# Kernel optimization log

Measured on AMD Instinct MI355X. Metric: run time of the kernel, lower is better.

The kernel has to match this reference:

```python
import jax, jax.numpy as jnp
import numpy as np

OMEGA = 0.3        # self.omega
NU = 0.2           # self.nu
LAMBDA_DECAY = 0.1 # lambda_decay
MU_INIT = 0.25     # nn.Parameter init
EPS_DENOM = 1e-8
EPS_SQRT = 1e-24   # safe sqrt (avoids nan grad at exactly-zero distance)


def setup_inputs() -> dict:
    key = jax.random.key(0)
    k1, k2, k3, k4 = jax.random.split(key, 4)
    T, D = 4096, 896  # seq_len, Qwen2.5-0.5B hidden size
    return {
        "hidden_states": jax.random.normal(k1, (T, D), dtype=jnp.float32),
        "m_t": jax.random.uniform(k2, (T,), dtype=jnp.float32),
        "c_t": jax.random.uniform(k3, (T,), dtype=jnp.float32),
        "d_t": jax.random.uniform(k4, (T,), dtype=jnp.float32),
        "mu": jnp.asarray(MU_INIT, dtype=jnp.float32),
    }


def _semantic_drift(hidden_states, m_t, c_t, d_t, mu):
    T, D = hidden_states.shape
    # F.normalize(h, p=2, dim=1): x / max(||x||, eps)
    norms = jnp.linalg.norm(hidden_states, axis=1, keepdims=True)
    h = hidden_states / jnp.maximum(norms, 1e-12)          # [T, D]

    # Causal decayed-softmax anchor: alpha[t, s] over s <= t
    sim = jnp.einsum("td,sd->ts", h, h)                    # [T, T], h(s)^T h(t) at row t
    idx = jnp.arange(T)
    tds = (idx[:, None] - idx[None, :]).astype(jnp.float32)  # t - s
    causal = tds >= 0.0
    sqrt_d = jnp.sqrt(jnp.asarray(D, jnp.float32))
    denom = sqrt_d * jnp.exp(LAMBDA_DECAY * tds) + EPS_DENOM
    logits = jnp.where(causal, sim / denom, -jnp.inf)
    alpha = jax.nn.softmax(logits, axis=1)                 # [T, T]
    g = jnp.einsum("ts,sd->td", alpha, h)                  # h_global(t), [T, D]

    # dist(h(t), h_global(t)) — normalize_hidden=True, so plain euclidean norm
    dist = jnp.sqrt(jnp.maximum(jnp.sum((h - g) ** 2, axis=1), EPS_SQRT))  # [T]

    # dist_max(t) = max_{s<=t} ||h(s) - h_global(t)|| (torch loop starts max at 0)
    hn2 = jnp.sum(h * h, axis=1)                           # [T]
    gn2 = jnp.sum(g * g, axis=1)                           # [T]
    cross = jnp.einsum("td,sd->ts", g, h)                  # g(t)·h(s)
    d2 = jnp.maximum(hn2[None, :] - 2.0 * cross + gn2[:, None], EPS_SQRT)
    dmat = jnp.sqrt(d2)                                    # [T, T], dist(h(s), g(t))
    dist_max = jnp.max(jnp.where(causal, dmat, 0.0), axis=1)
    dist_max = jnp.where(dist_max < 1e-6, 1.0, dist_max)

    dist_ratio = dist / (dist_max + EPS_DENOM)
    stability = 1.0 - OMEGA * c_t + NU * d_t
    xi = 1.0 - mu * m_t
    return jnp.clip(dist_ratio * stability * xi, 0.0, 1.0)  # [T]


def reference(hidden_states, m_t, c_t, d_t, mu):
    return _semantic_drift(hidden_states, m_t, c_t, d_t, mu)
```

## Files before the change

### kernel.cpp

```cpp
#include <hip/hip_runtime.h>
#include <math.h>


#define T_ 4096
#define D_ 896
#define TP (T_ + 64)

typedef float f32x4 __attribute__((ext_vector_type(4)));
typedef unsigned short u16x8 __attribute__((ext_vector_type(8)));
typedef __bf16 bf16x8 __attribute__((ext_vector_type(8)));

union V16 { uint4 u; u16x8 v; };

__device__ __forceinline__ u16x8 ld16(const unsigned short* p) {
  V16 x; x.u = *(const uint4*)p; return x.v;
}
__device__ __forceinline__ void st16(unsigned short* p, u16x8 v) {
  V16 x; x.v = v; *(uint4*)p = x.u;
}
__device__ __forceinline__ unsigned short f2bf(float f) {
  unsigned int u = __float_as_uint(f);
  u += 0x7FFFu + ((u >> 16) & 1u);
  return (unsigned short)(u >> 16);
}
__device__ __forceinline__ float bf2f(unsigned short b) {
  return __uint_as_float(((unsigned int)b) << 16);
}
__device__ __forceinline__ float4 bf4f(uint2 u) {
  return make_float4(bf2f((unsigned short)(u.x & 0xffff)),
                     bf2f((unsigned short)(u.x >> 16)),
                     bf2f((unsigned short)(u.y & 0xffff)),
                     bf2f((unsigned short)(u.y >> 16)));
}
__device__ __forceinline__ f32x4 mfma16(u16x8 a, u16x8 b, f32x4 c) {
  return __builtin_amdgcn_mfma_f32_16x16x32_bf16(
      __builtin_bit_cast(bf16x8, a), __builtin_bit_cast(bf16x8, b), c, 0, 0, 0);
}

typedef __attribute__((address_space(1))) const void glob_cv;
typedef __attribute__((address_space(3))) void lds_v;
__device__ __forceinline__ void gload16(const void* g, void* l) {
  __builtin_amdgcn_global_load_lds((glob_cv*)g, (lds_v*)l, 16, 0, 0);
}

__device__ __forceinline__ void stage32(const unsigned short* __restrict__ g0,
                                        int stride, unsigned short* lds0, int tid) {
  #pragma unroll
  for (int it = 0; it < 2; ++it) {
    const int e = it * 256 + tid;
    const int row = e >> 3, pg = e & 7;
    const int gg = pg ^ (row & 7);
    gload16(g0 + (size_t)row * stride + gg * 8, lds0 + e * 8);
  }
}

__device__ __forceinline__ void tri2_decode(int b, int& ti, int& sj) {
  int p = (int)((sqrtf(4.0f * (float)b + 1.0f) - 1.0f) * 0.5f);
  while ((p + 1) * (p + 2) <= b) ++p;
  while (p * (p + 1) > b) --p;
  const int r = b - p * (p + 1);
  if (r >= p + 1) { ti = 2 * p + 1; sj = r - (p + 1); }
  else            { ti = 2 * p;     sj = r; }
}

__global__ __launch_bounds__(256) void k_prep(const float* __restrict__ x,
    float* __restrict__ invnorm, unsigned short* __restrict__ hb) {
  const int t = (int)blockIdx.x, tid = (int)threadIdx.x;
  const int c = tid * 4;
  float4 v = make_float4(0.f, 0.f, 0.f, 0.f);
  float s = 0.f;
  if (c < D_) {
    v = *(const float4*)(x + (size_t)t * D_ + c);
    s = v.x * v.x + v.y * v.y + v.z * v.z + v.w * v.w;
  }
  __shared__ float sb[4];
  __shared__ float sinv;
  #pragma unroll
  for (int off = 32; off > 0; off >>= 1) s += __shfl_down(s, off, 64);
  if ((tid & 63) == 0) sb[tid >> 6] = s;
  __syncthreads();
  if (tid == 0) {
    const float tot = sb[0] + sb[1] + sb[2] + sb[3];
    const float iv = 1.0f / fmaxf(sqrtf(tot), 1e-12f);
    invnorm[t] = iv; sinv = iv;
  }
  __syncthreads();
  if (c < D_) {
    const float iv = sinv;
    *(ushort4*)(hb + (size_t)t * D_ + c) = make_ushort4(
        f2bf(v.x * iv), f2bf(v.y * iv), f2bf(v.z * iv), f2bf(v.w * iv));
  }
}

__global__ __launch_bounds__(256) void k_transp(const unsigned short* __restrict__ hb,
                                                unsigned short* __restrict__ hbTp) {
  __shared__ unsigned short Ts[32][36];
  const int t0 = (int)blockIdx.x * 32, d0 = (int)blockIdx.y * 32;
  const int r = (int)threadIdx.x >> 3, c = ((int)threadIdx.x & 7) * 4;
  const ushort4 v = *(const ushort4*)(hb + (size_t)(t0 + r) * D_ + d0 + c);
  Ts[r][c] = v.x; Ts[r][c + 1] = v.y; Ts[r][c + 2] = v.z; Ts[r][c + 3] = v.w;
  __syncthreads();
  const ushort4 o = make_ushort4(Ts[c][r], Ts[c + 1][r], Ts[c + 2][r], Ts[c + 3][r]);
  *(ushort4*)(hbTp + (size_t)(d0 + r) * TP + 32 + t0 + c) = o;
  if (blockIdx.x == 0)
    *(ushort4*)(hbTp + (size_t)(d0 + r) * TP + c) = make_ushort4(0, 0, 0, 0);
}

__global__ __launch_bounds__(256) void k_sega(const unsigned short* __restrict__ hb,
                                              float* __restrict__ Sseg) {
  const int seg = (int)blockIdx.x, tid = (int)threadIdx.x;
  const int wv = tid >> 6, lane = tid & 63;
  __shared__ float4 part[4][56];
  const int c = (int)blockIdx.y * 224 + lane * 4;
  float4 acc = make_float4(0.f, 0.f, 0.f, 0.f);
  if (lane < 56) {
    #pragma unroll
    for (int r = 0; r < 8; ++r) {
      const int row = seg * 32 + wv * 8 + r;
      const float4 h = bf4f(*(const uint2*)(hb + (size_t)row * D_ + c));
      acc.x += h.x; acc.y += h.y; acc.z += h.z; acc.w += h.w;
    }
    part[wv][lane] = acc;
  }
  __syncthreads();
  if (wv == 0 && lane < 56) {
    const float4 a = part[0][lane], b = part[1][lane];
    const float4 d = part[2][lane], e = part[3][lane];
    *(float4*)(Sseg + (size_t)seg * D_ + c) = make_float4(
        a.x + b.x + d.x + e.x, a.y + b.y + d.y + e.y,
        a.z + b.z + d.z + e.z, a.w + b.w + d.w + e.w);
  }
}

__global__ __launch_bounds__(256) void k_segb(const float* __restrict__ Sseg,
                                              float* __restrict__ Eseg) {
  const int tid = (int)threadIdx.x;
  const int wv = tid >> 6, lane = tid & 63;
  const int c = (int)blockIdx.x * 4 + wv;
  float v0 = Sseg[(size_t)lane * D_ + c];
  float v1 = Sseg[(size_t)(64 + lane) * D_ + c];
  const float o0 = v0, o1 = v1;
  #pragma unroll
  for (int off = 1; off < 64; off <<= 1) {
    const float n0 = __shfl_up(v0, off, 64);
    const float n1 = __shfl_up(v1, off, 64);
    if (lane >= off) { v0 += n0; v1 += n1; }
  }
  const float tot0 = __shfl(v0, 63, 64);
  Eseg[(size_t)lane * D_ + c] = v0 - o0;
  Eseg[(size_t)(64 + lane) * D_ + c] = v1 - o1 + tot0;
}

__global__ __launch_bounds__(64) void k_segc(const unsigned short* __restrict__ hb,
    const float* __restrict__ Eseg, float* __restrict__ P) {
  const int seg = (int)blockIdx.x, tid = (int)threadIdx.x;
  if (tid >= 56) return;
  const int c = (int)blockIdx.y * 224 + tid * 4;
  float4 run = *(const float4*)(Eseg + (size_t)seg * D_ + c);
  for (int r = 0; r < 32; ++r) {
    const int row = seg * 32 + r;
    const float4 h = bf4f(*(const uint2*)(hb + (size_t)row * D_ + c));
    run.x += h.x; run.y += h.y; run.z += h.z; run.w += h.w;
    *(float4*)(P + (size_t)row * D_ + c) = run;
  }
}

__global__ __launch_bounds__(256) void k_bandw(const unsigned short* __restrict__ hb,
    unsigned short* __restrict__ wband, float* __restrict__ invLb) {
  const int t0 = (int)blockIdx.x * 16;
  const int tid = (int)threadIdx.x;
  const int wv = tid >> 6, lane = tid & 63;
  const int tcol = lane & 15, quad = lane >> 4;
  __shared__ float sims[16][52];
  if (wv < 3) {
    const int s_base = t0 - 32 + wv * 16;
    if (s_base + 15 >= 0) {
      const int srow = max(s_base + tcol, 0);
      f32x4 acc = {};
      const unsigned short* arow = hb + (size_t)srow * D_ + quad * 8;
      const unsigned short* brow = hb + (size_t)(t0 + tcol) * D_ + quad * 8;
      #pragma unroll 1
      for (int c4 = 0; c4 < 4; ++c4) {
        u16x8 av[7], bv[7];
        #pragma unroll
        for (int i = 0; i < 7; ++i) {
          av[i] = ld16(arow + (c4 * 7 + i) * 32);
          bv[i] = ld16(brow + (c4 * 7 + i) * 32);
        }
        #pragma unroll
        for (int i = 0; i < 7; ++i) acc = mfma16(av[i], bv[i], acc);
      }
      #pragma unroll
      for (int r = 0; r < 4; ++r)
        sims[tcol][wv * 16 + quad * 4 + r] = acc[r];
    }
  }
  __syncthreads();
  if (wv == 0) {
    u16x8 af0, af1;
    float lsum = 0.f;
    #pragma unroll
    for (int j = 0; j < 8; ++j) {
      {
        const int k = quad * 8 + j;
        const int dt = tcol + 32 - k;
        const int s = t0 - 32 + k;
        unsigned short wb = 0;
        if (dt < 32 && s >= 0)
          wb = f2bf(__expf(sims[tcol][k] * (__expf(-0.1f * (float)dt) * 0.033407657f)));
        af0[j] = wb;
        lsum += bf2f(wb);
      }
      {
        const int k = 32 + quad * 8 + j;
        const int dt = tcol + 32 - k;
        unsigned short wb = 0;
        if (dt >= 0)
          wb = f2bf(__expf(sims[tcol][k] * (__expf(-0.1f * (float)dt) * 0.033407657f)));
        af1[j] = wb;
        lsum += bf2f(wb);
      }
    }
    lsum += __shfl_xor(lsum, 16, 64);
    lsum += __shfl_xor(lsum, 32, 64);
    st16(wband + (size_t)(t0 + tcol) * 64 + quad * 8, af0);
    st16(wband + (size_t)(t0 + tcol) * 64 + 32 + quad * 8, af1);
    if (lane < 16) {
      const int t = t0 + lane;
      invLb[t] = 1.0f / (lsum + ((t >= 32) ? (float)(t - 31) : 0.f));
    }
  }
}

__global__ __launch_bounds__(256) void k_bandg(const unsigned short* __restrict__ hbTp,
    const unsigned short* __restrict__ wband, const float* __restrict__ invLb,
    const float* __restrict__ P, const float* __restrict__ x,
    const float* __restrict__ invnorm, unsigned short* __restrict__ gb,
    float* __restrict__ gn2, float* __restrict__ dist2) {
  const int t0 = (int)blockIdx.x * 16;
  const int by = (int)blockIdx.y;
  const int tid = (int)threadIdx.x;
  const int wv = tid >> 6, lane = tid & 63;
  const int tcol = lane & 15, quad = lane >> 4;
  const u16x8 af0 = ld16(wband + (size_t)(t0 + tcol) * 64 + quad * 8);
  const u16x8 af1 = ld16(wband + (size_t)(t0 + tcol) * 64 + 32 + quad * 8);
  float invLr[4], inrr[4];
  #pragma unroll
  for (int r = 0; r < 4; ++r) {
    const int tt = t0 + quad * 4 + r;
    invLr[r] = invLb[tt];
    inrr[r]  = invnorm[tt];
  }
  float sgl[4] = {0.f, 0.f, 0.f, 0.f}, sdl[4] = {0.f, 0.f, 0.f, 0.f};
  for (int i = wv; i < 7; i += 4) {
    const int d = (by * 7 + i) * 16 + tcol;
    const unsigned short* brow = hbTp + (size_t)d * TP + t0 + quad * 8;
    const u16x8 b0 = ld16(brow);
    const u16x8 b1 = ld16(brow + 32);
    f32x4 C = {};
    C = mfma16(af0, b0, C);
    C = mfma16(af1, b1, C);
    #pragma unroll
    for (int r = 0; r < 4; ++r) {
      const int tt = t0 + quad * 4 + r;
      float gacc = C[r];
      if (tt >= 32) gacc += P[(size_t)(tt - 32) * D_ + d];
      const float g = gacc * invLr[r];
      gb[(size_t)tt * D_ + d] = f2bf(g);
      const float e = x[(size_t)tt * D_ + d] * inrr[r] - g;
      sgl[r] += g * g;
      sdl[r] += e * e;
    }
  }
  #pragma unroll
  for (int r = 0; r < 4; ++r) {
    float sg = sgl[r], sd = sdl[r];
    sg += __shfl_xor(sg, 1, 64); sg += __shfl_xor(sg, 2, 64);
    sg += __shfl_xor(sg, 4, 64); sg += __shfl_xor(sg, 8, 64);
    sd += __shfl_xor(sd, 1, 64); sd += __shfl_xor(sd, 2, 64);
    sd += __shfl_xor(sd, 4, 64); sd += __shfl_xor(sd, 8, 64);
    if (tcol == 0) {
      atomicAdd(&gn2[t0 + quad * 4 + r], sg);
      atomicAdd(&dist2[t0 + quad * 4 + r], sd);
    }
  }
}

__global__ __launch_bounds__(256, 5) void k_gemm3(const unsigned short* __restrict__ gb,
    const unsigned short* __restrict__ hb, const float* __restrict__ gn2,
    unsigned int* __restrict__ dmaxu) {
  const int bswz = ((int)blockIdx.x & 7) * 132 + ((int)blockIdx.x >> 3);
  int ti, sj;
  tri2_decode(bswz, ti, sj);
  const int t0 = ti * 64, s0 = sj * 128;
  __shared__ unsigned short As[64 * 64];
  __shared__ unsigned short Bs[128 * 64];
  __shared__ unsigned int dmx[64];
  const int tid = (int)threadIdx.x;
  const int lane = tid & 63, wv = tid >> 6;
  const int tcol = lane & 15, quad = lane >> 4;
  if (tid < 64) dmx[tid] = 0u;
  f32x4 acc[4][2] = {};

  for (int kc = 0; kc < 14; ++kc) {
    __syncthreads();
    stage32(gb + (size_t)t0 * D_ + kc * 64, D_, As, tid);
    stage32(hb + (size_t)s0 * D_ + kc * 64, D_, Bs, tid);
    stage32(hb + (size_t)(s0 + 64) * D_ + kc * 64, D_, Bs + 64 * 64, tid);
    __syncthreads();
    #pragma unroll
    for (int ks = 0; ks < 2; ++ks) {
      const int go = ((ks * 4 + quad) ^ (tcol & 7)) * 8;
      u16x8 bf[2], af[4];
      #pragma unroll
      for (int ni = 0; ni < 2; ++ni)
        bf[ni] = ld16(&Bs[(wv * 32 + ni * 16 + tcol) * 64 + go]);
      #pragma unroll
      for (int mi = 0; mi < 4; ++mi)
        af[mi] = ld16(&As[(mi * 16 + tcol) * 64 + go]);
      #pragma unroll
      for (int mi = 0; mi < 4; ++mi)
        #pragma unroll
        for (int ni = 0; ni < 2; ++ni)
          acc[mi][ni] = mfma16(af[mi], bf[ni], acc[mi][ni]);
    }
  }

  #pragma unroll
  for (int mi = 0; mi < 4; ++mi) {
    #pragma unroll
    for (int r = 0; r < 4; ++r) {
      const int t = t0 + mi * 16 + quad * 4 + r;
      const float gn = gn2[t];
      float m2 = 0.f;
      #pragma unroll
      for (int ni = 0; ni < 2; ++ni) {
        const int s = s0 + wv * 32 + ni * 16 + tcol;
        if (t >= s)
          m2 = fmaxf(m2, fmaxf(1.0f - 2.0f * acc[mi][ni][r] + gn, 1e-24f));
      }
      m2 = fmaxf(m2, __shfl_xor(m2, 1, 64));
      m2 = fmaxf(m2, __shfl_xor(m2, 2, 64));
      m2 = fmaxf(m2, __shfl_xor(m2, 4, 64));
      m2 = fmaxf(m2, __shfl_xor(m2, 8, 64));
      if (tcol == 0 && m2 > 0.f)
        atomicMax(&dmx[mi * 16 + quad * 4 + r], __float_as_uint(m2));
    }
  }
  __syncthreads();
  if (tid < 64) {
    const unsigned int v = dmx[tid];
    if (v) atomicMax(&dmaxu[t0 + tid], v);
  }
}

__global__ __launch_bounds__(256) void k_final(const float* __restrict__ m_t,
    const float* __restrict__ c_t, const float* __restrict__ d_t,
    const float* __restrict__ mu, const float* __restrict__ dist2,
    const unsigned int* __restrict__ dmaxu, float* __restrict__ out) {
  const int t = (int)blockIdx.x * 256 + (int)threadIdx.x;
  if (t >= T_) return;
  float ratio;
  if (t == 0) {
    ratio = 0.f;
  } else {
    float dmax = sqrtf(__uint_as_float(dmaxu[t]));
    if (dmax < 1e-6f) dmax = 1.0f;
    ratio = sqrtf(fmaxf(dist2[t], 1e-24f)) / (dmax + 1e-8f);
  }
  const float stab = 1.0f - 0.3f * c_t[t] + 0.2f * d_t[t];
  const float xi = 1.0f - mu[0] * m_t[t];
  out[t] = fminf(fmaxf(ratio * stab * xi, 0.f), 1.f);
}

extern "C" void kernel_launch(void* const* d_in, const int* in_sizes, int n_in,
                              void* d_out, int out_size, void* d_ws, size_t ws_size,
                              hipStream_t stream) {
  const float* x   = (const float*)d_in[0];
  const float* m_t = (const float*)d_in[1];
  const float* c_t = (const float*)d_in[2];
  const float* d_t = (const float*)d_in[3];
  const float* mu  = (const float*)d_in[4];
  float* out = (float*)d_out;

  float* ws = (float*)d_ws;
  float* invnorm = ws;
  unsigned int* dmaxu = (unsigned int*)(ws + (size_t)T_);
  float* gn2     = ws + 2 * (size_t)T_;
  float* dist2   = ws + 3 * (size_t)T_;
  float* invLb   = ws + 4 * (size_t)T_;
  float* Sseg    = ws + 5 * (size_t)T_;
  float* Eseg    = Sseg + 128 * (size_t)D_;
  float* P       = Eseg + 128 * (size_t)D_;
  unsigned short* hb    = (unsigned short*)(P + (size_t)T_ * D_);
  unsigned short* hbTp  = hb + (size_t)T_ * D_;
  unsigned short* gb    = hbTp + (size_t)D_ * TP;
  unsigned short* wband = gb + (size_t)T_ * D_;

  hipMemsetAsync(dmaxu, 0, 3 * (size_t)T_ * sizeof(unsigned int), stream);

  k_prep<<<T_, 256, 0, stream>>>(x, invnorm, hb);
  k_transp<<<dim3(T_ / 32, D_ / 32), 256, 0, stream>>>(hb, hbTp);
  k_sega<<<dim3(128, 4), 256, 0, stream>>>(hb, Sseg);
  k_segb<<<224, 256, 0, stream>>>(Sseg, Eseg);
  k_segc<<<dim3(128, 4), 64, 0, stream>>>(hb, Eseg, P);
  k_bandw<<<T_ / 16, 256, 0, stream>>>(hb, wband, invLb);
  k_bandg<<<dim3(T_ / 16, 8), 256, 0, stream>>>(hbTp, wband, invLb, P, x, invnorm,
                                                gb, gn2, dist2);
  k_gemm3<<<1056, 256, 0, stream>>>(gb, hb, gn2, dmaxu);
  k_final<<<(T_ + 255) / 256, 256, 0, stream>>>(m_t, c_t, d_t, mu, dist2, dmaxu, out);
}
```

Baseline: 141.8 us.

## Use 2-wave 64x128 tiles in gemm3 and halve prefix-sum segment length

The distance-max GEMM now runs with 128 threads (2 waves), and each wave computes a 64x64 sub-tile (4x4 MFMA accumulators) instead of 64x32 with 4 waves. The A fragments loaded from LDS are reused across more MFMAs, at the cost of more registers per thread and lower thread-level parallelism. Separately, the segmented prefix sum over hidden states switches from 128 segments of 32 rows to 256 segments of 16 rows. That shortens the serial per-thread scan in k_segc and widens its grid, while the segment scan kernel handles 4 chunks per lane.

```diff
diff --git a/kernel.cpp b/kernel.cpp
--- a/kernel.cpp
+++ b/kernel.cpp
@@ -48,6 +48,18 @@
   #pragma unroll
   for (int it = 0; it < 2; ++it) {
     const int e = it * 256 + tid;
+    const int row = e >> 3, pg = e & 7;
+    const int gg = pg ^ (row & 7);
+    gload16(g0 + (size_t)row * stride + gg * 8, lds0 + e * 8);
+  }
+}
+
+template <int ITERS>
+__device__ __forceinline__ void stage128t(const unsigned short* __restrict__ g0,
+                                          int stride, unsigned short* lds0, int tid) {
+  #pragma unroll
+  for (int it = 0; it < ITERS; ++it) {
+    const int e = it * 128 + tid;
     const int row = e >> 3, pg = e & 7;
     const int gg = pg ^ (row & 7);
     gload16(g0 + (size_t)row * stride + gg * 8, lds0 + e * 8);
@@ -115,8 +127,8 @@
   float4 acc = make_float4(0.f, 0.f, 0.f, 0.f);
   if (lane < 56) {
     #pragma unroll
-    for (int r = 0; r < 8; ++r) {
-      const int row = seg * 32 + wv * 8 + r;
+    for (int r = 0; r < 4; ++r) {
+      const int row = seg * 16 + wv * 4 + r;
       const float4 h = bf4f(*(const uint2*)(hb + (size_t)row * D_ + c));
       acc.x += h.x; acc.y += h.y; acc.z += h.z; acc.w += h.w;
     }
@@ -139,16 +151,24 @@
   const int c = (int)blockIdx.x * 4 + wv;
   float v0 = Sseg[(size_t)lane * D_ + c];
   float v1 = Sseg[(size_t)(64 + lane) * D_ + c];
-  const float o0 = v0, o1 = v1;
+  float v2 = Sseg[(size_t)(128 + lane) * D_ + c];
+  float v3 = Sseg[(size_t)(192 + lane) * D_ + c];
+  const float o0 = v0, o1 = v1, o2 = v2, o3 = v3;
   #pragma unroll
   for (int off = 1; off < 64; off <<= 1) {
     const float n0 = __shfl_up(v0, off, 64);
     const float n1 = __shfl_up(v1, off, 64);
-    if (lane >= off) { v0 += n0; v1 += n1; }
+    const float n2 = __shfl_up(v2, off, 64);
+    const float n3 = __shfl_up(v3, off, 64);
+    if (lane >= off) { v0 += n0; v1 += n1; v2 += n2; v3 += n3; }
   }
   const float tot0 = __shfl(v0, 63, 64);
+  const float tot1 = __shfl(v1, 63, 64);
+  const float tot2 = __shfl(v2, 63, 64);
   Eseg[(size_t)lane * D_ + c] = v0 - o0;
   Eseg[(size_t)(64 + lane) * D_ + c] = v1 - o1 + tot0;
+  Eseg[(size_t)(128 + lane) * D_ + c] = v2 - o2 + (tot0 + tot1);
+  Eseg[(size_t)(192 + lane) * D_ + c] = v3 - o3 + (tot0 + tot1 + tot2);
 }
 
 __global__ __launch_bounds__(64) void k_segc(const unsigned short* __restrict__ hb,
@@ -157,8 +177,8 @@
   if (tid >= 56) return;
   const int c = (int)blockIdx.y * 224 + tid * 4;
   float4 run = *(const float4*)(Eseg + (size_t)seg * D_ + c);
-  for (int r = 0; r < 32; ++r) {
-    const int row = seg * 32 + r;
+  for (int r = 0; r < 16; ++r) {
+    const int row = seg * 16 + r;
     const float4 h = bf4f(*(const uint2*)(hb + (size_t)row * D_ + c));
     run.x += h.x; run.y += h.y; run.z += h.z; run.w += h.w;
     *(float4*)(P + (size_t)row * D_ + c) = run;
@@ -286,7 +306,7 @@
   }
 }
 
-__global__ __launch_bounds__(256, 5) void k_gemm3(const unsigned short* __restrict__ gb,
+__global__ __launch_bounds__(128, 3) void k_gemm3(const unsigned short* __restrict__ gb,
     const unsigned short* __restrict__ hb, const float* __restrict__ gn2,
     unsigned int* __restrict__ dmaxu) {
   const int bswz = ((int)blockIdx.x & 7) * 132 + ((int)blockIdx.x >> 3);
@@ -300,28 +320,27 @@
   const int lane = tid & 63, wv = tid >> 6;
   const int tcol = lane & 15, quad = lane >> 4;
   if (tid < 64) dmx[tid] = 0u;
-  f32x4 acc[4][2] = {};
+  f32x4 acc[4][4] = {};
 
   for (int kc = 0; kc < 14; ++kc) {
     __syncthreads();
-    stage32(gb + (size_t)t0 * D_ + kc * 64, D_, As, tid);
-    stage32(hb + (size_t)s0 * D_ + kc * 64, D_, Bs, tid);
-    stage32(hb + (size_t)(s0 + 64) * D_ + kc * 64, D_, Bs + 64 * 64, tid);
+    stage128t<4>(gb + (size_t)t0 * D_ + kc * 64, D_, As, tid);
+    stage128t<8>(hb + (size_t)s0 * D_ + kc * 64, D_, Bs, tid);
     __syncthreads();
     #pragma unroll
     for (int ks = 0; ks < 2; ++ks) {
       const int go = ((ks * 4 + quad) ^ (tcol & 7)) * 8;
-      u16x8 bf[2], af[4];
-      #pragma unroll
-      for (int ni = 0; ni < 2; ++ni)
-        bf[ni] = ld16(&Bs[(wv * 32 + ni * 16 + tcol) * 64 + go]);
+      u16x8 af[4], bf[4];
       #pragma unroll
       for (int mi = 0; mi < 4; ++mi)
         af[mi] = ld16(&As[(mi * 16 + tcol) * 64 + go]);
       #pragma unroll
+      for (int ni = 0; ni < 4; ++ni)
+        bf[ni] = ld16(&Bs[(wv * 64 + ni * 16 + tcol) * 64 + go]);
+      #pragma unroll
       for (int mi = 0; mi < 4; ++mi)
         #pragma unroll
-        for (int ni = 0; ni < 2; ++ni)
+        for (int ni = 0; ni < 4; ++ni)
           acc[mi][ni] = mfma16(af[mi], bf[ni], acc[mi][ni]);
     }
   }
@@ -334,8 +353,8 @@
       const float gn = gn2[t];
       float m2 = 0.f;
       #pragma unroll
-      for (int ni = 0; ni < 2; ++ni) {
-        const int s = s0 + wv * 32 + ni * 16 + tcol;
+      for (int ni = 0; ni < 4; ++ni) {
+        const int s = s0 + wv * 64 + ni * 16 + tcol;
         if (t >= s)
           m2 = fmaxf(m2, fmaxf(1.0f - 2.0f * acc[mi][ni][r] + gn, 1e-24f));
       }
@@ -390,8 +409,8 @@
   float* dist2   = ws + 3 * (size_t)T_;
   float* invLb   = ws + 4 * (size_t)T_;
   float* Sseg    = ws + 5 * (size_t)T_;
-  float* Eseg    = Sseg + 128 * (size_t)D_;
-  float* P       = Eseg + 128 * (size_t)D_;
+  float* Eseg    = Sseg + 256 * (size_t)D_;
+  float* P       = Eseg + 256 * (size_t)D_;
   unsigned short* hb    = (unsigned short*)(P + (size_t)T_ * D_);
   unsigned short* hbTp  = hb + (size_t)T_ * D_;
   unsigned short* gb    = hbTp + (size_t)D_ * TP;
@@ -401,12 +420,12 @@
 
   k_prep<<<T_, 256, 0, stream>>>(x, invnorm, hb);
   k_transp<<<dim3(T_ / 32, D_ / 32), 256, 0, stream>>>(hb, hbTp);
-  k_sega<<<dim3(128, 4), 256, 0, stream>>>(hb, Sseg);
+  k_sega<<<dim3(256, 4), 256, 0, stream>>>(hb, Sseg);
   k_segb<<<224, 256, 0, stream>>>(Sseg, Eseg);
-  k_segc<<<dim3(128, 4), 64, 0, stream>>>(hb, Eseg, P);
+  k_segc<<<dim3(256, 4), 64, 0, stream>>>(hb, Eseg, P);
   k_bandw<<<T_ / 16, 256, 0, stream>>>(hb, wband, invLb);
   k_bandg<<<dim3(T_ / 16, 8), 256, 0, stream>>>(hbTp, wband, invLb, P, x, invnorm,
                                                 gb, gn2, dist2);
-  k_gemm3<<<1056, 256, 0, stream>>>(gb, hb, gn2, dmaxu);
+  k_gemm3<<<1056, 128, 0, stream>>>(gb, hb, gn2, dmaxu);
   k_final<<<(T_ + 255) / 256, 256, 0, stream>>>(m_t, c_t, d_t, mu, dist2, dmaxu, out);
 }
```

New measurement: 143.3 us. About the same (+1.0%).

## Fuse normalize, transpose and segment sums; compute prefix sums inline in band kernel

Applied to the files above, without the earlier changes.

Merges the normalization, transpose and per-segment column sum kernels into one kernel that stages 32 rows in shared memory. The segment size drops to 16 rows to match the band kernel's tile. The materialized full prefix-sum matrix P is removed, so the band kernel rebuilds each prefix from the segment exclusive sum plus the 16 transposed values it loads. This cuts three launches and a large fp32 write/read, at the cost of redundant per-lane prefix work and a large shared buffer that limits occupancy.

```diff
diff --git a/kernel.cpp b/kernel.cpp
--- a/kernel.cpp
+++ b/kernel.cpp
@@ -5,6 +5,7 @@
 #define T_ 4096
 #define D_ 896
 #define TP (T_ + 64)
+#define PSTR 900
 
 typedef float f32x4 __attribute__((ext_vector_type(4)));
 typedef unsigned short u16x8 __attribute__((ext_vector_type(8)));
@@ -25,12 +26,6 @@
 }
 __device__ __forceinline__ float bf2f(unsigned short b) {
   return __uint_as_float(((unsigned int)b) << 16);
-}
-__device__ __forceinline__ float4 bf4f(uint2 u) {
-  return make_float4(bf2f((unsigned short)(u.x & 0xffff)),
-                     bf2f((unsigned short)(u.x >> 16)),
-                     bf2f((unsigned short)(u.y & 0xffff)),
-                     bf2f((unsigned short)(u.y >> 16)));
 }
 __device__ __forceinline__ f32x4 mfma16(u16x8 a, u16x8 b, f32x4 c) {
   return __builtin_amdgcn_mfma_f32_16x16x32_bf16(
@@ -63,72 +58,81 @@
   else            { ti = 2 * p;     sj = r; }
 }
 
-__global__ __launch_bounds__(256) void k_prep(const float* __restrict__ x,
-    float* __restrict__ invnorm, unsigned short* __restrict__ hb) {
-  const int t = (int)blockIdx.x, tid = (int)threadIdx.x;
-  const int c = tid * 4;
-  float4 v = make_float4(0.f, 0.f, 0.f, 0.f);
-  float s = 0.f;
-  if (c < D_) {
-    v = *(const float4*)(x + (size_t)t * D_ + c);
-    s = v.x * v.x + v.y * v.y + v.z * v.z + v.w * v.w;
-  }
-  __shared__ float sb[4];
-  __shared__ float sinv;
-  #pragma unroll
-  for (int off = 32; off > 0; off >>= 1) s += __shfl_down(s, off, 64);
-  if ((tid & 63) == 0) sb[tid >> 6] = s;
+__global__ __launch_bounds__(256, 2) void k_prep2(const float* __restrict__ x,
+    float* __restrict__ invnorm, unsigned short* __restrict__ hb,
+    unsigned short* __restrict__ hbTp, float* __restrict__ Sseg) {
+  __shared__ unsigned short Ts[32 * PSTR];
+  const int b = (int)blockIdx.x;
+  const int t0 = b * 32;
+  const int tid = (int)threadIdx.x, wv = tid >> 6, lane = tid & 63;
+
+  float4 v[8][4];
+  #pragma unroll
+  for (int rr = 0; rr < 8; ++rr) {
+    const int t = t0 + wv * 8 + rr;
+    #pragma unroll
+    for (int k = 0; k < 4; ++k) {
+      const int c4 = lane + 64 * k;
+      if (k < 3 || lane < 32)
+        v[rr][k] = *(const float4*)(x + (size_t)t * D_ + c4 * 4);
+    }
+  }
+  #pragma unroll
+  for (int rr = 0; rr < 8; ++rr) {
+    const int row = wv * 8 + rr;
+    const int t = t0 + row;
+    float s = 0.f;
+    #pragma unroll
+    for (int k = 0; k < 4; ++k)
+      if (k < 3 || lane < 32)
+        s += v[rr][k].x * v[rr][k].x + v[rr][k].y * v[rr][k].y +
+             v[rr][k].z * v[rr][k].z + v[rr][k].w * v[rr][k].w;
+    #pragma unroll
+    for (int off = 32; off > 0; off >>= 1) s += __shfl_down(s, off, 64);
+    const float iv = 1.0f / fmaxf(sqrtf(__shfl(s, 0, 64)), 1e-12f);
+    if (lane == 0) invnorm[t] = iv;
+    #pragma unroll
+    for (int k = 0; k < 4; ++k) {
+      const int c4 = lane + 64 * k;
+      if (k < 3 || lane < 32) {
+        const ushort4 o = make_ushort4(f2bf(v[rr][k].x * iv), f2bf(v[rr][k].y * iv),
+                                       f2bf(v[rr][k].z * iv), f2bf(v[rr][k].w * iv));
+        *(ushort4*)(hb + (size_t)t * D_ + c4 * 4) = o;
+        *(ushort4*)(&Ts[row * PSTR + c4 * 4]) = o;
+      }
+    }
+  }
   __syncthreads();
-  if (tid == 0) {
-    const float tot = sb[0] + sb[1] + sb[2] + sb[3];
-    const float iv = 1.0f / fmaxf(sqrtf(tot), 1e-12f);
-    invnorm[t] = iv; sinv = iv;
-  }
-  __syncthreads();
-  if (c < D_) {
-    const float iv = sinv;
-    *(ushort4*)(hb + (size_t)t * D_ + c) = make_ushort4(
-        f2bf(v.x * iv), f2bf(v.y * iv), f2bf(v.z * iv), f2bf(v.w * iv));
-  }
-}
-
-__global__ __launch_bounds__(256) void k_transp(const unsigned short* __restrict__ hb,
-                                                unsigned short* __restrict__ hbTp) {
-  __shared__ unsigned short Ts[32][36];
-  const int t0 = (int)blockIdx.x * 32, d0 = (int)blockIdx.y * 32;
-  const int r = (int)threadIdx.x >> 3, c = ((int)threadIdx.x & 7) * 4;
-  const ushort4 v = *(const ushort4*)(hb + (size_t)(t0 + r) * D_ + d0 + c);
-  Ts[r][c] = v.x; Ts[r][c + 1] = v.y; Ts[r][c + 2] = v.z; Ts[r][c + 3] = v.w;
-  __syncthreads();
-  const ushort4 o = make_ushort4(Ts[c][r], Ts[c + 1][r], Ts[c + 2][r], Ts[c + 3][r]);
-  *(ushort4*)(hbTp + (size_t)(d0 + r) * TP + 32 + t0 + c) = o;
-  if (blockIdx.x == 0)
-    *(ushort4*)(hbTp + (size_t)(d0 + r) * TP + c) = make_ushort4(0, 0, 0, 0);
-}
-
-__global__ __launch_bounds__(256) void k_sega(const unsigned short* __restrict__ hb,
-                                              float* __restrict__ Sseg) {
-  const int seg = (int)blockIdx.x, tid = (int)threadIdx.x;
-  const int wv = tid >> 6, lane = tid & 63;
-  __shared__ float4 part[4][56];
-  const int c = (int)blockIdx.y * 224 + lane * 4;
-  float4 acc = make_float4(0.f, 0.f, 0.f, 0.f);
-  if (lane < 56) {
-    #pragma unroll
-    for (int r = 0; r < 8; ++r) {
-      const int row = seg * 32 + wv * 8 + r;
-      const float4 h = bf4f(*(const uint2*)(hb + (size_t)row * D_ + c));
-      acc.x += h.x; acc.y += h.y; acc.z += h.z; acc.w += h.w;
-    }
-    part[wv][lane] = acc;
-  }
-  __syncthreads();
-  if (wv == 0 && lane < 56) {
-    const float4 a = part[0][lane], b = part[1][lane];
-    const float4 d = part[2][lane], e = part[3][lane];
-    *(float4*)(Sseg + (size_t)seg * D_ + c) = make_float4(
-        a.x + b.x + d.x + e.x, a.y + b.y + d.y + e.y,
-        a.z + b.z + d.z + e.z, a.w + b.w + d.w + e.w);
+
+  for (int c = tid; c < D_; c += 256) {
+    #pragma unroll
+    for (int half = 0; half < 2; ++half) {
+      float segsum = 0.f;
+      #pragma unroll
+      for (int q = 0; q < 4; ++q) {
+        float gs = 0.f;
+        #pragma unroll
+        for (int r = 0; r < 4; ++r)
+          gs += bf2f(Ts[(half * 16 + q * 4 + r) * PSTR + c]);
+        segsum += gs;
+      }
+      Sseg[(size_t)(2 * b + half) * D_ + c] = segsum;
+    }
+  }
+
+  const int r = tid >> 3, c = (tid & 7) * 4;
+  #pragma unroll 4
+  for (int dt = 0; dt < 28; ++dt) {
+    const int d = dt * 32 + r;
+    const ushort4 o = make_ushort4(Ts[c * PSTR + d], Ts[(c + 1) * PSTR + d],
+                                   Ts[(c + 2) * PSTR + d], Ts[(c + 3) * PSTR + d]);
+    *(ushort4*)(hbTp + (size_t)d * TP + 32 + t0 + c) = o;
+  }
+  if (b == 0) {
+    for (int e = tid; e < D_ * 8; e += 256) {
+      const int d = e >> 3, cc = (e & 7) * 4;
+      *(ushort4*)(hbTp + (size_t)d * TP + cc) = make_ushort4(0, 0, 0, 0);
+    }
   }
 }
 
@@ -139,30 +143,24 @@
   const int c = (int)blockIdx.x * 4 + wv;
   float v0 = Sseg[(size_t)lane * D_ + c];
   float v1 = Sseg[(size_t)(64 + lane) * D_ + c];
-  const float o0 = v0, o1 = v1;
+  float v2 = Sseg[(size_t)(128 + lane) * D_ + c];
+  float v3 = Sseg[(size_t)(192 + lane) * D_ + c];
+  const float o0 = v0, o1 = v1, o2 = v2, o3 = v3;
   #pragma unroll
   for (int off = 1; off < 64; off <<= 1) {
     const float n0 = __shfl_up(v0, off, 64);
     const float n1 = __shfl_up(v1, off, 64);
-    if (lane >= off) { v0 += n0; v1 += n1; }
+    const float n2 = __shfl_up(v2, off, 64);
+    const float n3 = __shfl_up(v3, off, 64);
+    if (lane >= off) { v0 += n0; v1 += n1; v2 += n2; v3 += n3; }
   }
   const float tot0 = __shfl(v0, 63, 64);
+  const float tot1 = __shfl(v1, 63, 64);
+  const float tot2 = __shfl(v2, 63, 64);
   Eseg[(size_t)lane * D_ + c] = v0 - o0;
   Eseg[(size_t)(64 + lane) * D_ + c] = v1 - o1 + tot0;
-}
-
-__global__ __launch_bounds__(64) void k_segc(const unsigned short* __restrict__ hb,
-    const float* __restrict__ Eseg, float* __restrict__ P) {
-  const int seg = (int)blockIdx.x, tid = (int)threadIdx.x;
-  if (tid >= 56) return;
-  const int c = (int)blockIdx.y * 224 + tid * 4;
-  float4 run = *(const float4*)(Eseg + (size_t)seg * D_ + c);
-  for (int r = 0; r < 32; ++r) {
-    const int row = seg * 32 + r;
-    const float4 h = bf4f(*(const uint2*)(hb + (size_t)row * D_ + c));
-    run.x += h.x; run.y += h.y; run.z += h.z; run.w += h.w;
-    *(float4*)(P + (size_t)row * D_ + c) = run;
-  }
+  Eseg[(size_t)(128 + lane) * D_ + c] = v2 - o2 + (tot0 + tot1);
+  Eseg[(size_t)(192 + lane) * D_ + c] = v3 - o3 + (tot0 + tot1 + tot2);
 }
 
 __global__ __launch_bounds__(256) void k_bandw(const unsigned short* __restrict__ hb,
@@ -234,7 +232,7 @@
 
 __global__ __launch_bounds__(256) void k_bandg(const unsigned short* __restrict__ hbTp,
     const unsigned short* __restrict__ wband, const float* __restrict__ invLb,
-    const float* __restrict__ P, const float* __restrict__ x,
+    const float* __restrict__ Eseg, const float* __restrict__ x,
     const float* __restrict__ invnorm, unsigned short* __restrict__ gb,
     float* __restrict__ gn2, float* __restrict__ dist2) {
   const int t0 = (int)blockIdx.x * 16;
@@ -244,6 +242,7 @@
   const int tcol = lane & 15, quad = lane >> 4;
   const u16x8 af0 = ld16(wband + (size_t)(t0 + tcol) * 64 + quad * 8);
   const u16x8 af1 = ld16(wband + (size_t)(t0 + tcol) * 64 + 32 + quad * 8);
+  const int sg = (t0 >> 4) - 2;
   float invLr[4], inrr[4];
   #pragma unroll
   for (int r = 0; r < 4; ++r) {
@@ -260,11 +259,27 @@
     f32x4 C = {};
     C = mfma16(af0, b0, C);
     C = mfma16(af1, b1, C);
+    float pr[4] = {0.f, 0.f, 0.f, 0.f};
+    if (t0 >= 32) {
+      const unsigned short* prow = hbTp + (size_t)d * TP + t0;
+      const uint4 w0 = *(const uint4*)prow;
+      const uint4 w1 = *(const uint4*)(prow + 8);
+      const unsigned int wz[8] = {w0.x, w0.y, w0.z, w0.w, w1.x, w1.y, w1.z, w1.w};
+      float run = Eseg[(size_t)sg * D_ + d];
+      #pragma unroll
+      for (int jj = 0; jj < 16; ++jj) {
+        const unsigned int uu = wz[jj >> 1];
+        const unsigned short hh =
+            (jj & 1) ? (unsigned short)(uu >> 16) : (unsigned short)(uu & 0xffffu);
+        run += bf2f(hh);
+        if ((jj >> 2) == quad) pr[jj & 3] = run;
+      }
+    }
     #pragma unroll
     for (int r = 0; r < 4; ++r) {
       const int tt = t0 + quad * 4 + r;
       float gacc = C[r];
-      if (tt >= 32) gacc += P[(size_t)(tt - 32) * D_ + d];
+      if (tt >= 32) gacc += pr[r];
       const float g = gacc * invLr[r];
       gb[(size_t)tt * D_ + d] = f2bf(g);
       const float e = x[(size_t)tt * D_ + d] * inrr[r] - g;
@@ -274,13 +289,13 @@
   }
   #pragma unroll
   for (int r = 0; r < 4; ++r) {
-    float sg = sgl[r], sd = sdl[r];
-    sg += __shfl_xor(sg, 1, 64); sg += __shfl_xor(sg, 2, 64);
-    sg += __shfl_xor(sg, 4, 64); sg += __shfl_xor(sg, 8, 64);
+    float sg2 = sgl[r], sd = sdl[r];
+    sg2 += __shfl_xor(sg2, 1, 64); sg2 += __shfl_xor(sg2, 2, 64);
+    sg2 += __shfl_xor(sg2, 4, 64); sg2 += __shfl_xor(sg2, 8, 64);
     sd += __shfl_xor(sd, 1, 64); sd += __shfl_xor(sd, 2, 64);
     sd += __shfl_xor(sd, 4, 64); sd += __shfl_xor(sd, 8, 64);
     if (tcol == 0) {
-      atomicAdd(&gn2[t0 + quad * 4 + r], sg);
+      atomicAdd(&gn2[t0 + quad * 4 + r], sg2);
       atomicAdd(&dist2[t0 + quad * 4 + r], sd);
     }
   }
@@ -390,8 +405,8 @@
   float* dist2   = ws + 3 * (size_t)T_;
   float* invLb   = ws + 4 * (size_t)T_;
   float* Sseg    = ws + 5 * (size_t)T_;
-  float* Eseg    = Sseg + 128 * (size_t)D_;
-  float* P       = Eseg + 128 * (size_t)D_;
+  float* Eseg    = Sseg + 256 * (size_t)D_;
+  float* P       = Eseg + 256 * (size_t)D_;
   unsigned short* hb    = (unsigned short*)(P + (size_t)T_ * D_);
   unsigned short* hbTp  = hb + (size_t)T_ * D_;
   unsigned short* gb    = hbTp + (size_t)D_ * TP;
@@ -399,13 +414,10 @@
 
   hipMemsetAsync(dmaxu, 0, 3 * (size_t)T_ * sizeof(unsigned int), stream);
 
-  k_prep<<<T_, 256, 0, stream>>>(x, invnorm, hb);
-  k_transp<<<dim3(T_ / 32, D_ / 32), 256, 0, stream>>>(hb, hbTp);
-  k_sega<<<dim3(128, 4), 256, 0, stream>>>(hb, Sseg);
+  k_prep2<<<T_ / 32, 256, 0, stream>>>(x, invnorm, hb, hbTp, Sseg);
   k_segb<<<224, 256, 0, stream>>>(Sseg, Eseg);
-  k_segc<<<dim3(128, 4), 64, 0, stream>>>(hb, Eseg, P);
   k_bandw<<<T_ / 16, 256, 0, stream>>>(hb, wband, invLb);
-  k_bandg<<<dim3(T_ / 16, 8), 256, 0, stream>>>(hbTp, wband, invLb, P, x, invnorm,
+  k_bandg<<<dim3(T_ / 16, 8), 256, 0, stream>>>(hbTp, wband, invLb, Eseg, x, invnorm,
                                                 gb, gn2, dist2);
   k_gemm3<<<1056, 256, 0, stream>>>(gb, hb, gn2, dmaxu);
   k_final<<<(T_ + 255) / 256, 256, 0, stream>>>(m_t, c_t, d_t, mu, dist2, dmaxu, out);
```

Measured after the change: 142.4 us. About the same (+0.4%).
